# Kernel optimization log

Measured on AMD Instinct MI355X. Metric: run time of the kernel, lower is better.

## Reference

```python
import jax, jax.numpy as jnp
from jax import lax
import numpy as np

# Problem dims (see init_kwargs)
B, CIN, H, W = 4, 128, 128, 128
COUT, K, STRIDE, PAD, DIL, GROUPS, OG = 128, 3, 1, 1, 1, 1, 2


def setup_inputs() -> dict:
    key = jax.random.key(0)
    k0, k1, k2 = jax.random.split(key, 3)
    x = jax.random.normal(k0, (B, CIN, H, W), dtype=jnp.float32)
    off_ch = 3 * OG * K * K  # with_mask=True -> scale=3 (dy, dx, mask)
    # Small random offset-conv weights so offsets are non-trivial (zero-init would degenerate to plain conv)
    w_off = jax.random.normal(k1, (off_ch, CIN, K, K), dtype=jnp.float32) * 0.01
    b_off = jnp.zeros((off_ch,), jnp.float32)
    stdv = 1.0 / np.sqrt(CIN * K * K)
    weight = jax.random.uniform(k2, (COUT, CIN // GROUPS, K, K), jnp.float32, -stdv, stdv)
    bias = jnp.zeros((COUT,), jnp.float32)
    return {"x": x, "w_off": w_off, "b_off": b_off, "weight": weight, "bias": bias}


def _deform_conv2d(x, offset, mask, weight, bias):
    # x: [B,C,H,W]; offset: [B,2*OG*K2,Ho,Wo]; mask: [B,OG*K2,Ho,Wo]
    Bn, C, Hn, Wn = x.shape
    O = weight.shape[0]
    K2 = K * K
    Ho = (Hn + 2 * PAD - DIL * (K - 1) - 1) // STRIDE + 1
    Wo = (Wn + 2 * PAD - DIL * (K - 1) - 1) // STRIDE + 1
    # torchvision layout: per offset group, per kernel point, (dy, dx) interleaved
    off = offset.reshape(Bn, OG, K2, 2, Ho, Wo)
    kg = (jnp.arange(K) * DIL).astype(x.dtype)
    kyf = jnp.repeat(kg, K)  # [K2] kernel row offset, k2 = i*K + j
    kxf = jnp.tile(kg, K)    # [K2] kernel col offset
    base_y = (jnp.arange(Ho) * STRIDE - PAD).astype(x.dtype)
    base_x = (jnp.arange(Wo) * STRIDE - PAD).astype(x.dtype)
    # sampling coords: [B,OG,K2,Ho,Wo]
    sy = base_y[None, None, None, :, None] + kyf[None, None, :, None, None] + off[:, :, :, 0]
    sx = base_x[None, None, None, None, :] + kxf[None, None, :, None, None] + off[:, :, :, 1]
    y0f = jnp.floor(sy)
    x0f = jnp.floor(sx)
    ly = sy - y0f  # bilinear fractional weights
    lx = sx - x0f
    y0 = y0f.astype(jnp.int32)
    x0 = x0f.astype(jnp.int32)
    Cg = C // OG
    xg = x.reshape(Bn, OG, Cg, Hn * Wn)

    def gather(iy, ix):
        # zero-padding semantics: out-of-range corners contribute 0
        valid = ((iy >= 0) & (iy < Hn) & (ix >= 0) & (ix < Wn)).astype(x.dtype)
        idx = (jnp.clip(iy, 0, Hn - 1) * Wn + jnp.clip(ix, 0, Wn - 1)).reshape(Bn, OG, 1, -1)
        v = jnp.take_along_axis(xg, idx, axis=3).reshape(Bn, OG, Cg, K2, Ho, Wo)
        return v * valid[:, :, None]

    v00 = gather(y0, x0)
    v01 = gather(y0, x0 + 1)
    v10 = gather(y0 + 1, x0)
    v11 = gather(y0 + 1, x0 + 1)
    wy = ly[:, :, None]  # broadcast over channel dim
    wx = lx[:, :, None]
    val = (v00 * (1 - wy) * (1 - wx) + v01 * (1 - wy) * wx
           + v10 * wy * (1 - wx) + v11 * wy * wx)
    # modulated DCNv2: multiply sampled values by sigmoid mask
    val = val * mask.reshape(Bn, OG, 1, K2, Ho, Wo)
    # im2col GEMM: cols [B,G,(C/G)*K2,Ho*Wo] x weight [G,O/G,(C/G)*K2]
    cols = val.reshape(Bn, GROUPS, (C // GROUPS) * K2, Ho * Wo)
    wg = weight.reshape(GROUPS, O // GROUPS, (C // GROUPS) * K2)
    out = jnp.einsum('gok,bgkn->bgon', wg, cols).reshape(Bn, O, Ho, Wo)
    return out + bias[None, :, None, None]


def reference(x, w_off, b_off, weight, bias):
    off_out = lax.conv_general_dilated(
        x, w_off, (STRIDE, STRIDE), [(PAD, PAD), (PAD, PAD)],
        rhs_dilation=(DIL, DIL), dimension_numbers=('NCHW', 'OIHW', 'NCHW')
    ) + b_off[None, :, None, None]
    oh, ow, m = jnp.split(off_out, 3, axis=1)
    offset = jnp.concatenate([oh, ow], axis=1)
    mask = jax.nn.sigmoid(m)
    return _deform_conv2d(x, offset, mask, weight, bias)
```

## Files before the change

kernel.cpp:

```cpp
#include <hip/hip_runtime.h>
#include <math.h>

#define NB 4
#define NC 128
#define NH 128
#define NW 128
#define NHW (NH*NW)
#define NCOUT 128

#define SY_OFF 0
#define SX_OFF 1179648
#define MK_OFF 2359296
#define WOFF_OFF 3538944
#define WMAIN_OFF 3580416
#define XT_OFF 3663360

typedef short short8 __attribute__((ext_vector_type(8)));
typedef float f32x4 __attribute__((ext_vector_type(4)));
typedef float f32x2 __attribute__((ext_vector_type(2)));

__device__ inline short f2bf(float f) {
    unsigned u = __float_as_uint(f);
    u = (u + 0x7FFFu + ((u >> 16) & 1u)) >> 16;
    return (short)u;
}
__device__ inline unsigned pack2(float lo, float hi) {
    unsigned r;
    asm("v_cvt_pk_bf16_f32 %0, %1, %2" : "=v"(r) : "v"(lo), "v"(hi));
    return r;
}
__device__ inline unsigned pkf16(float a, float b) {
    auto h = __builtin_amdgcn_cvt_pkrtz(a, b);
    unsigned r; __builtin_memcpy(&r, &h, 4); return r;
}
__device__ inline float f16f(unsigned s) {
    unsigned short us = (unsigned short)s;
    __fp16 h; __builtin_memcpy(&h, &us, 2); return (float)h;
}
__device__ inline f32x2 pkmul(f32x2 a, f32x2 b) {
    f32x2 d; asm("v_pk_mul_f32 %0, %1, %2" : "=v"(d) : "v"(a), "v"(b)); return d;
}
__device__ inline f32x2 pkfma(f32x2 a, f32x2 b, f32x2 c) {
    f32x2 d; asm("v_pk_fma_f32 %0, %1, %2, %3" : "=v"(d) : "v"(a), "v"(b), "v"(c)); return d;
}
__device__ inline f32x2 cpair(unsigned u) {
    f32x2 c; c.x = __uint_as_float(u << 16); c.y = __uint_as_float(u); return c;
}
__device__ inline void gload_lds16(const void* g, void* l) {
    __builtin_amdgcn_global_load_lds(
        (const __attribute__((address_space(1))) unsigned int*)g,
        (__attribute__((address_space(3))) unsigned int*)l, 16, 0, 0);
}

__global__ void wtrans_kernel(const float* __restrict__ w_off,
                              const float* __restrict__ weight,
                              float* __restrict__ ws)
{
    int i = blockIdx.x * 256 + threadIdx.x;
    if (i < 36*2304) {
        int s = i / 2304, rem = i - s*2304;
        int row = rem / 36, c = rem - row*36;
        int chunk = s / 9, k2 = s - 9*chunk;
        float v = (row < 54 && c < 32) ? w_off[(row*NC + chunk*32 + c)*9 + k2] : 0.f;
        ((short*)(ws + WOFF_OFF))[i] = f2bf(v);
    } else if (i < 36*2304 + 36*4608) {
        int j = i - 36*2304;
        int s = j / 4608, rem = j - s*4608;
        int row = rem / 36, c = rem - row*36;
        int chunk = s / 9, k2 = s - 9*chunk;
        float v = (c < 32) ? weight[(row*NC + chunk*32 + c)*9 + k2] : 0.f;
        ((short*)(ws + WMAIN_OFF))[j] = f2bf(v);
    }
}

__global__ __launch_bounds__(256) void xtrans_kernel(
    const float* __restrict__ x, float* __restrict__ ws)
{
    short* xT = (short*)(ws + XT_OFF);
    const int bid = blockIdx.x;
    const int ys = bid & 15, cg = (bid >> 4) & 15, b = bid >> 8;
    const int col = threadIdx.x & 127, rr = threadIdx.x >> 7;
    const float* xb = x + ((long)(b*NC + cg*8))*NHW;
#pragma unroll
    for (int yy = 0; yy < 4; ++yy) {
        const int y = ys*8 + yy*2 + rr;
        const float* p = xb + y*NW + col;
        float v[8];
#pragma unroll
        for (int q = 0; q < 8; ++q) v[q] = p[q*NHW];
        uint4 u = make_uint4(pack2(v[0],v[1]), pack2(v[2],v[3]),
                             pack2(v[4],v[5]), pack2(v[6],v[7]));
        *(uint4*)&xT[(((long)(b*16+cg)*NH + y)*NW + col)*8] = u;
    }
}

__global__ __launch_bounds__(512, 4) void offconv_kernel(
    float* __restrict__ ws, const float* __restrict__ b_off)
{
    __shared__ short wslab[2][2304];
    int bid = blockIdx.x;
    bid = (bid & 7) * 64 + (bid >> 3);
    const int b   = bid >> 7;
    const int ho  = bid & 127;
    const int tid = threadIdx.x;
    const int lane = tid & 63;
    const int wid = tid >> 6;
    const int n = lane & 15, g = lane >> 4;
    const int px = wid*16 + n;
    const short* woff = (const short*)(ws + WOFF_OFF);
    const char*  xTb  = (const char*)((const short*)(ws + XT_OFF) + (long)b*16*NHW*8);

    f32x4 acc[4];
#pragma unroll
    for (int rf = 0; rf < 4; ++rf) acc[rf] = (f32x4){0.f,0.f,0.f,0.f};

    auto DMA = [&](int it, int buf) {
        if (tid < 288) gload_lds16(woff + it*2304 + tid*8, &wslab[buf][tid*8]);
    };
    auto LOADB = [&](int it) -> short8 {
        const int chunk = it/9, k2 = it - 9*chunk;
        const int y = ho + k2/3 - 1, xc = px + (k2%3) - 1;
        short8 bf = (short8){0,0,0,0,0,0,0,0};
        if ((unsigned)y < NH && (unsigned)xc < NW)
            bf = *(const short8*)(xTb + ((long)(chunk*4 + g)*NHW + y*NW + xc)*16);
        return bf;
    };

    DMA(0, 0);
    short8 bcur = LOADB(0);
    __syncthreads();

#pragma unroll 1
    for (int it = 0; it < 36; ++it) {
        const int cur = it & 1, nxt = cur ^ 1;
        short8 bnext;
        if (it < 35) { DMA(it+1, nxt); bnext = LOADB(it+1); }
        __builtin_amdgcn_sched_barrier(0);
#pragma unroll
        for (int rf = 0; rf < 4; ++rf) {
            short8 af = *(const short8*)&wslab[cur][(rf*16 + n)*36 + 8*g];
            acc[rf] = __builtin_amdgcn_mfma_f32_16x16x32_bf16(af, bcur, acc[rf], 0,0,0);
        }
        __syncthreads();
        bcur = bnext;
    }

#pragma unroll
    for (int rf = 0; rf < 4; ++rf) {
#pragma unroll
        for (int r = 0; r < 4; ++r) {
            int cout = 16*rf + 4*g + r;
            if (cout >= 54) continue;
            float v = acc[rf][r] + b_off[cout];
            if (cout < 36) {
                int og = cout / 18, rem = cout - 18*og;
                int k2c = rem >> 1, d = cout & 1;
                float base = d ? (float)(px - 1 + (k2c % 3))
                              : (float)(ho - 1 + (k2c / 3));
                ws[(d ? SX_OFF : SY_OFF) + (((b*2+og)*9 + k2c)*NHW) + ho*NW + px] = v + base;
            } else {
                int cc = cout - 36;
                int og = cc / 9, k2c = cc - 9*og;
                ws[MK_OFF + (((b*2+og)*9 + k2c)*NHW) + ho*NW + px] = 1.f/(1.f+expf(-v));
            }
        }
    }
}

__global__ __launch_bounds__(512, 2) void deform_kernel(
    float* __restrict__ ws, const float* __restrict__ bias,
    float* __restrict__ out)
{
    __shared__ short4 pI[9][128];
    __shared__ uint2  pWp[9][128];
    __shared__ short  slabs[9][4608];

    int bid = blockIdx.x;
    bid = (bid & 7) * 64 + (bid >> 3);
    const int b   = bid >> 7;
    const int ho  = bid & 127;
    const int tid = threadIdx.x;
    const int lane = tid & 63;
    const int wid = tid >> 6;
    const int n = lane & 15, g = lane >> 4;
    const int pxl = 16*wid + n;
    const short* wmn = (const short*)(ws + WMAIN_OFF);
    const char*  xTb = (const char*)((const short*)(ws + XT_OFF) + (long)b*16*NHW*8);

    f32x4 acc[8];
#pragma unroll
    for (int rf = 0; rf < 8; ++rf) acc[rf] = (f32x4){0.f,0.f,0.f,0.f};

    auto DMAC = [&](int chunk) {
        const short* src = wmn + chunk*9*4608;
        short* dst = &slabs[0][0];
#pragma unroll 1
        for (int u = tid; u < 5184; u += 512)
            gload_lds16(src + u*8, dst + u*8);
    };

#define GLOAD(chunk, k2, G0, G1, G2, G3) do {                           \
        const short4 I_ = pI[(k2)][pxl];                                \
        const char* xp_ = xTb + (long)((chunk)*4 + g)*(NHW*16);         \
        G0 = *(const uint4*)(xp_ + (((int)I_.x) << 4));                 \
        G1 = *(const uint4*)(xp_ + (((int)I_.y) << 4));                 \
        G2 = *(const uint4*)(xp_ + (((int)I_.z) << 4));                 \
        G3 = *(const uint4*)(xp_ + (((int)I_.w) << 4));                 \
    } while (0)

#define FIN(k2, G0, G1, G2, G3, Adst) do {                              \
        const uint2 wp_ = *(const uint2*)&pWp[(k2)][pxl];               \
        const float w0s = f16f(wp_.x), w1s = f16f(wp_.x >> 16);         \
        const float w2s = f16f(wp_.y), w3s = f16f(wp_.y >> 16);         \
        const f32x2 W0_ = {w0s, w0s}, W1_ = {w1s, w1s};                 \
        const f32x2 W2_ = {w2s, w2s}, W3_ = {w3s, w3s};                 \
        uint4 u_; unsigned* up_ = (unsigned*)&u_;                       \
        const unsigned* a_ = (const unsigned*)&G0;                      \
        const unsigned* b_ = (const unsigned*)&G1;                      \
        const unsigned* c_ = (const unsigned*)&G2;                      \
        const unsigned* d_ = (const unsigned*)&G3;                      \
        _Pragma("unroll")                                               \
        for (int e = 0; e < 4; ++e) {                                   \
            f32x2 r_ = pkmul(cpair(d_[e]), W3_);                        \
            r_ = pkfma(cpair(c_[e]), W2_, r_);                          \
            r_ = pkfma(cpair(b_[e]), W1_, r_);                          \
            r_ = pkfma(cpair(a_[e]), W0_, r_);                          \
            up_[e] = pack2(r_.x, r_.y);                                 \
        }                                                               \
        __builtin_memcpy(&Adst, &u_, 16);                               \
    } while (0)

#define MFMA8(Ain, k2) do {                                             \
        _Pragma("unroll")                                               \
        for (int rf = 0; rf < 8; ++rf) {                                \
            short8 bf = *(const short8*)&slabs[(k2)][(16*rf + n)*36 + 8*g]; \
            acc[rf] = __builtin_amdgcn_mfma_f32_16x16x32_bf16(Ain, bf, acc[rf], 0,0,0); \
        }                                                               \
    } while (0)

#define PBODY(k2, chunk, Ain, Aout, H0,H1,H2,H3, F0,F1,F2,F3) do {      \
        if ((k2) < 7) GLOAD(chunk, (k2)+2, F0, F1, F2, F3);             \
        MFMA8(Ain, k2);                                                 \
        if ((k2) < 8) FIN((k2)+1, H0, H1, H2, H3, Aout);                \
    } while (0)

    uint4 Ga0, Ga1, Ga2, Ga3, Gb0, Gb1, Gb2, Gb3;
    short8 Acur, Anxt;

#pragma unroll 1
    for (int og = 0; og < 2; ++og) {
        if (og) __syncthreads();
        DMAC(og*2);
        for (int e = tid; e < 1152; e += 512) {
            const int row = e >> 7, p = e & 127;
            const int sidx = (((b*2+og)*9 + row)*NHW) + ho*NW + p;
            const float sy = ws[SY_OFF + sidx];
            const float sx = ws[SX_OFF + sidx];
            const float m  = ws[MK_OFF + sidx];
            const float y0f = floorf(sy), x0f = floorf(sx);
            const float ly = sy - y0f, lx = sx - x0f;
            const int y0 = (int)y0f, x0i = (int)x0f;
            const int y1 = y0 + 1, x1 = x0i + 1;
            const bool vy0 = (unsigned)y0 < NH, vy1 = (unsigned)y1 < NH;
            const bool vx0 = (unsigned)x0i < NW, vx1 = (unsigned)x1 < NW;
            const int cy0 = min(max(y0,0),NH-1), cy1 = min(max(y1,0),NH-1);
            const int cx0 = min(max(x0i,0),NW-1), cx1 = min(max(x1,0),NW-1);
            pI[row][p] = make_short4(
                (short)(cy0*NW + cx0), (short)(cy0*NW + cx1),
                (short)(cy1*NW + cx0), (short)(cy1*NW + cx1));
            const float W0 = (vy0 && vx0) ? (1.f-ly)*(1.f-lx)*m : 0.f;
            const float W1 = (vy0 && vx1) ? (1.f-ly)*lx*m       : 0.f;
            const float W2 = (vy1 && vx0) ? ly*(1.f-lx)*m       : 0.f;
            const float W3 = (vy1 && vx1) ? ly*lx*m             : 0.f;
            pWp[row][p] = make_uint2(pkf16(W0, W1), pkf16(W2, W3));
        }
        __syncthreads();

#pragma unroll 1
        for (int cc = 0; cc < 2; ++cc) {
            const int chunk = og*2 + cc;
            if (cc) {
                __syncthreads();
                DMAC(chunk);
                asm volatile("s_waitcnt vmcnt(0) lgkmcnt(0)" ::: "memory");
                __builtin_amdgcn_s_barrier();
                __builtin_amdgcn_sched_barrier(0);
            }
            GLOAD(chunk, 0, Ga0, Ga1, Ga2, Ga3);
            FIN(0, Ga0, Ga1, Ga2, Ga3, Acur);
            GLOAD(chunk, 1, Gb0, Gb1, Gb2, Gb3);
            PBODY(0, chunk, Acur, Anxt, Gb0,Gb1,Gb2,Gb3, Ga0,Ga1,Ga2,Ga3);
            PBODY(1, chunk, Anxt, Acur, Ga0,Ga1,Ga2,Ga3, Gb0,Gb1,Gb2,Gb3);
            PBODY(2, chunk, Acur, Anxt, Gb0,Gb1,Gb2,Gb3, Ga0,Ga1,Ga2,Ga3);
            PBODY(3, chunk, Anxt, Acur, Ga0,Ga1,Ga2,Ga3, Gb0,Gb1,Gb2,Gb3);
            PBODY(4, chunk, Acur, Anxt, Gb0,Gb1,Gb2,Gb3, Ga0,Ga1,Ga2,Ga3);
            PBODY(5, chunk, Anxt, Acur, Ga0,Ga1,Ga2,Ga3, Gb0,Gb1,Gb2,Gb3);
            PBODY(6, chunk, Acur, Anxt, Gb0,Gb1,Gb2,Gb3, Ga0,Ga1,Ga2,Ga3);
            PBODY(7, chunk, Anxt, Acur, Ga0,Ga1,Ga2,Ga3, Gb0,Gb1,Gb2,Gb3);
            PBODY(8, chunk, Acur, Anxt, Gb0,Gb1,Gb2,Gb3, Ga0,Ga1,Ga2,Ga3);
        }
    }
#undef PBODY
#undef MFMA8
#undef GLOAD
#undef FIN

#pragma unroll
    for (int rf = 0; rf < 8; ++rf) {
        const int cout = 16*rf + n;
        const float bb = bias[cout];
        float4 o = make_float4(acc[rf][0]+bb, acc[rf][1]+bb,
                               acc[rf][2]+bb, acc[rf][3]+bb);
        *(float4*)&out[((b*NCOUT + cout)*NH + ho)*NW + 16*wid + 4*g] = o;
    }
}

extern "C" void kernel_launch(void* const* d_in, const int* in_sizes, int n_in,
                              void* d_out, int out_size, void* d_ws, size_t ws_size,
                              hipStream_t stream)
{
    const float* x      = (const float*)d_in[0];
    const float* w_off  = (const float*)d_in[1];
    const float* b_off  = (const float*)d_in[2];
    const float* weight = (const float*)d_in[3];
    const float* bias   = (const float*)d_in[4];
    float* out = (float*)d_out;
    float* ws  = (float*)d_ws;

    hipLaunchKernelGGL(wtrans_kernel, dim3(972), dim3(256), 0, stream,
                       w_off, weight, ws);
    hipLaunchKernelGGL(xtrans_kernel, dim3(1024), dim3(256), 0, stream,
                       x, ws);
    hipLaunchKernelGGL(offconv_kernel, dim3(NB*NH), dim3(512), 0, stream,
                       ws, b_off);
    hipLaunchKernelGGL(deform_kernel, dim3(NB*NH), dim3(512), 0, stream,
                       ws, bias, out);
}
```

Baseline: 93.30 us.

## Stage input row window in LDS for bilinear gathers and double-buffer weight slabs

Each block now copies an 8-row window of the channel-chunked bf16 input (rows ho-3..ho+4, with zero-padded edges) into shared memory, so the four bilinear corner reads come from LDS instead of scattered global loads. A precomputed packed LDS index per sample carries a flag that falls back to global loads when a corner lies outside the window. The full 9-slab weight staging is replaced by a two-buffer ring that streams one kernel-point slab per k2 step. In exchange the explicit register software pipeline is dropped and a barrier is added per k2 step, and the shared-memory footprint changes, which may lower occupancy.

```diff
diff --git a/kernel.cpp b/kernel.cpp
--- a/kernel.cpp
+++ b/kernel.cpp
@@ -171,9 +171,11 @@
     float* __restrict__ ws, const float* __restrict__ bias,
     float* __restrict__ out)
 {
-    __shared__ short4 pI[9][128];
-    __shared__ uint2  pWp[9][128];
-    __shared__ short  slabs[9][4608];
+    __shared__ short4   pI[9][128];
+    __shared__ unsigned pL[9][128];
+    __shared__ uint2    pWp[9][128];
+    __shared__ short    xc[33792];
+    __shared__ short    wslab[2][4608];
 
     int bid = blockIdx.x;
     bid = (bid & 7) * 64 + (bid >> 3);
@@ -191,21 +193,47 @@
 #pragma unroll
     for (int rf = 0; rf < 8; ++rf) acc[rf] = (f32x4){0.f,0.f,0.f,0.f};
 
-    auto DMAC = [&](int chunk) {
-        const short* src = wmn + chunk*9*4608;
-        short* dst = &slabs[0][0];
-#pragma unroll 1
-        for (int u = tid; u < 5184; u += 512)
-            gload_lds16(src + u*8, dst + u*8);
+    auto DMA = [&](int slabIdx, int buf) {
+        const short* src = wmn + slabIdx*4608;
+        gload_lds16(src + tid*8, &wslab[buf][tid*8]);
+        if (tid < 64) gload_lds16(src + 4096 + tid*8, &wslab[buf][4096 + tid*8]);
     };
-
-#define GLOAD(chunk, k2, G0, G1, G2, G3) do {                           \
-        const short4 I_ = pI[(k2)][pxl];                                \
-        const char* xp_ = xTb + (long)((chunk)*4 + g)*(NHW*16);         \
-        G0 = *(const uint4*)(xp_ + (((int)I_.x) << 4));                 \
-        G1 = *(const uint4*)(xp_ + (((int)I_.y) << 4));                 \
-        G2 = *(const uint4*)(xp_ + (((int)I_.z) << 4));                 \
-        G3 = *(const uint4*)(xp_ + (((int)I_.w) << 4));                 \
+    auto XSTAGE = [&](int chunk) {
+#pragma unroll 1
+        for (int u = tid; u < 4096; u += 512) {
+            const int slot = u >> 9, rem = u & 511;
+            const int gx = rem >> 2, pl = rem & 3;
+            const int gy = min(max(ho - 3 + slot, 0), NH-1);
+            const short* src = (const short*)xTb +
+                ((long)(chunk*4 + pl)*NHW + gy*NW + gx)*8;
+            gload_lds16(src, &xc[((slot*132 + gx + 2)*4 + pl)*8]);
+        }
+    };
+
+    for (int u = tid; u < 128; u += 512) {
+        const int slot = u >> 4, e = (u >> 2) & 3, pl = u & 3;
+        const int lpx = (e < 2) ? e : (128 + e);
+        *(uint4*)&xc[((slot*132 + lpx)*4 + pl)*8] = make_uint4(0,0,0,0);
+    }
+
+#define GLOADL(k2, chunk, G0, G1, G2, G3) do {                          \
+        const unsigned pv_ = pL[(k2)][pxl];                             \
+        const unsigned i0_ = pv_ & 0xFFFFu;                             \
+        const unsigned i1_ = (pv_ >> 16) & 0x7FFFu;                     \
+        const short* b0_ = &xc[(i0_*4 + g)*8];                          \
+        const short* b1_ = &xc[(i1_*4 + g)*8];                          \
+        G0 = *(const uint4*)b0_;                                        \
+        G1 = *(const uint4*)(b0_ + 32);     \
+        G2 = *(const uint4*)b1_;                                        \
+        G3 = *(const uint4*)(b1_ + 32);                                 \
+        if (__builtin_expect((pv_ >> 31) != 0, 0)) {                    \
+            const short4 I_ = pI[(k2)][pxl];                            \
+            const char* xp_ = xTb + (long)((chunk)*4 + g)*(NHW*16);     \
+            G0 = *(const uint4*)(xp_ + (((int)I_.x) << 4));             \
+            G1 = *(const uint4*)(xp_ + (((int)I_.y) << 4));             \
+            G2 = *(const uint4*)(xp_ + (((int)I_.z) << 4));             \
+            G3 = *(const uint4*)(xp_ + (((int)I_.w) << 4));             \
+        }                                                               \
     } while (0)
 
 #define FIN(k2, G0, G1, G2, G3, Adst) do {                              \
@@ -230,27 +258,20 @@
         __builtin_memcpy(&Adst, &u_, 16);                               \
     } while (0)
 
-#define MFMA8(Ain, k2) do {                                             \
+#define MFMA8(Ain, buf) do {                                            \
         _Pragma("unroll")                                               \
         for (int rf = 0; rf < 8; ++rf) {                                \
-            short8 bf = *(const short8*)&slabs[(k2)][(16*rf + n)*36 + 8*g]; \
+            short8 bf = *(const short8*)&wslab[(buf)][(16*rf + n)*36 + 8*g]; \
             acc[rf] = __builtin_amdgcn_mfma_f32_16x16x32_bf16(Ain, bf, acc[rf], 0,0,0); \
         }                                                               \
     } while (0)
 
-#define PBODY(k2, chunk, Ain, Aout, H0,H1,H2,H3, F0,F1,F2,F3) do {      \
-        if ((k2) < 7) GLOAD(chunk, (k2)+2, F0, F1, F2, F3);             \
-        MFMA8(Ain, k2);                                                 \
-        if ((k2) < 8) FIN((k2)+1, H0, H1, H2, H3, Aout);                \
-    } while (0)
-
-    uint4 Ga0, Ga1, Ga2, Ga3, Gb0, Gb1, Gb2, Gb3;
-    short8 Acur, Anxt;
+    uint4 G0, G1, G2, G3;
+    short8 A;
 
 #pragma unroll 1
     for (int og = 0; og < 2; ++og) {
-        if (og) __syncthreads();
-        DMAC(og*2);
+        __syncthreads();
         for (int e = tid; e < 1152; e += 512) {
             const int row = e >> 7, p = e & 127;
             const int sidx = (((b*2+og)*9 + row)*NHW) + ho*NW + p;
@@ -268,6 +289,14 @@
             pI[row][p] = make_short4(
                 (short)(cy0*NW + cx0), (short)(cy0*NW + cx1),
                 (short)(cy1*NW + cx0), (short)(cy1*NW + cx1));
+            const int basex = min(max(x0i, -1), NW-1);
+            int s0 = cy0 - ho + 3, s1 = cy1 - ho + 3;
+            const unsigned flag =
+                ((unsigned)s0 > 7u || (unsigned)s1 > 7u) ? (1u << 31) : 0u;
+            s0 = min(max(s0, 0), 7); s1 = min(max(s1, 0), 7);
+            const unsigned i0 = (unsigned)(s0*132 + basex + 2);
+            const unsigned i1 = (unsigned)(s1*132 + basex + 2);
+            pL[row][p] = i0 | (i1 << 16) | flag;
             const float W0 = (vy0 && vx0) ? (1.f-ly)*(1.f-lx)*m : 0.f;
             const float W1 = (vy0 && vx1) ? (1.f-ly)*lx*m       : 0.f;
             const float W2 = (vy1 && vx0) ? ly*(1.f-lx)*m       : 0.f;
@@ -279,31 +308,31 @@
 #pragma unroll 1
         for (int cc = 0; cc < 2; ++cc) {
             const int chunk = og*2 + cc;
-            if (cc) {
-                __syncthreads();
-                DMAC(chunk);
-                asm volatile("s_waitcnt vmcnt(0) lgkmcnt(0)" ::: "memory");
-                __builtin_amdgcn_s_barrier();
-                __builtin_amdgcn_sched_barrier(0);
+            if (cc) __syncthreads();
+            XSTAGE(chunk);
+            DMA(chunk*9, 0);
+            asm volatile("s_waitcnt vmcnt(0) lgkmcnt(0)" ::: "memory");
+            __builtin_amdgcn_s_barrier();
+            __builtin_amdgcn_sched_barrier(0);
+
+#pragma unroll 1
+            for (int k2 = 0; k2 < 9; ++k2) {
+                const int buf = k2 & 1;
+                if (k2 < 8) DMA(chunk*9 + k2 + 1, buf ^ 1);
+                GLOADL(k2, chunk, G0, G1, G2, G3);
+                FIN(k2, G0, G1, G2, G3, A);
+                MFMA8(A, buf);
+                if (k2 < 8) {
+                    asm volatile("s_waitcnt vmcnt(0) lgkmcnt(0)" ::: "memory");
+                    __builtin_amdgcn_s_barrier();
+                    __builtin_amdgcn_sched_barrier(0);
+                }
             }
-            GLOAD(chunk, 0, Ga0, Ga1, Ga2, Ga3);
-            FIN(0, Ga0, Ga1, Ga2, Ga3, Acur);
-            GLOAD(chunk, 1, Gb0, Gb1, Gb2, Gb3);
-            PBODY(0, chunk, Acur, Anxt, Gb0,Gb1,Gb2,Gb3, Ga0,Ga1,Ga2,Ga3);
-            PBODY(1, chunk, Anxt, Acur, Ga0,Ga1,Ga2,Ga3, Gb0,Gb1,Gb2,Gb3);
-            PBODY(2, chunk, Acur, Anxt, Gb0,Gb1,Gb2,Gb3, Ga0,Ga1,Ga2,Ga3);
-            PBODY(3, chunk, Anxt, Acur, Ga0,Ga1,Ga2,Ga3, Gb0,Gb1,Gb2,Gb3);
-            PBODY(4, chunk, Acur, Anxt, Gb0,Gb1,Gb2,Gb3, Ga0,Ga1,Ga2,Ga3);
-            PBODY(5, chunk, Anxt, Acur, Ga0,Ga1,Ga2,Ga3, Gb0,Gb1,Gb2,Gb3);
-            PBODY(6, chunk, Acur, Anxt, Gb0,Gb1,Gb2,Gb3, Ga0,Ga1,Ga2,Ga3);
-            PBODY(7, chunk, Anxt, Acur, Ga0,Ga1,Ga2,Ga3, Gb0,Gb1,Gb2,Gb3);
-            PBODY(8, chunk, Acur, Anxt, Gb0,Gb1,Gb2,Gb3, Ga0,Ga1,Ga2,Ga3);
-        }
-    }
-#undef PBODY
+        }
+    }
+#undef GLOADL
+#undef FIN
 #undef MFMA8
-#undef GLOAD
-#undef FIN
 
 #pragma unroll
     for (int rf = 0; rf < 8; ++rf) {
```

Result: slower. 130.8 us (+40.1%).
